# Performance work log

Hardware: AMD Instinct MI355X
Metric: run time of the kernel (lower is better)

## Reference

```python
import jax, jax.numpy as jnp
import numpy as np

N_SRC = 50000
N_DST = 50000
N_EDGES = 500000
HIDDEN = 128
HEADS = 8
HEAD_DIM = HIDDEN // HEADS
SCALE = HEAD_DIM ** -0.5


def setup_inputs() -> dict:
    key = jax.random.key(0)
    ks = jax.random.split(key, 12)
    lim = 1.0 / np.sqrt(HIDDEN)
    def lin(k):
        kw, kb = jax.random.split(k)
        W = jax.random.uniform(kw, (HIDDEN, HIDDEN), jnp.float32, -lim, lim)
        b = jax.random.uniform(kb, (HIDDEN,), jnp.float32, -lim, lim)
        return W, b
    Wq, bq = lin(ks[0]); Wk, bk = lin(ks[1]); Wv, bv = lin(ks[2]); Wo, bo = lin(ks[3])
    return {
        "x_src": jax.random.normal(ks[4], (N_SRC, HIDDEN), jnp.float32),
        "x_dst": jax.random.normal(ks[5], (N_DST, HIDDEN), jnp.float32),
        "edge_index": jax.random.randint(ks[6], (2, N_EDGES), 0, N_SRC, jnp.int64),
        "Wq": Wq, "bq": bq, "Wk": Wk, "bk": bk, "Wv": Wv, "bv": bv,
        "Wo": Wo, "bo": bo,
        "edge_bias": jax.random.normal(ks[7], (HEADS,), jnp.float32) * 0.02,
    }


def reference(x_src, x_dst, edge_index, Wq, bq, Wk, bk, Wv, bv, Wo, bo, edge_bias):
    num_dst = x_dst.shape[0]
    # projections (torch Linear: y = x W^T + b), reshape to (N, H, D)
    q = (x_dst @ Wq.T + bq).reshape(num_dst, HEADS, HEAD_DIM)
    k = (x_src @ Wk.T + bk).reshape(-1, HEADS, HEAD_DIM)
    v = (x_src @ Wv.T + bv).reshape(-1, HEADS, HEAD_DIM)
    src_idx, dst_idx = edge_index[0], edge_index[1]
    # per-edge dot-product scores: (E, H)
    scores = (q[dst_idx] * k[src_idx]).sum(-1) * SCALE + edge_bias
    # sparse softmax over edges grouped by destination
    m = jax.ops.segment_max(scores, dst_idx, num_segments=num_dst)  # (N_dst, H)
    e = jnp.exp(scores - m[dst_idx])
    s = jax.ops.segment_sum(e, dst_idx, num_segments=num_dst)  # (N_dst, H)
    w = e / (s[dst_idx] + 1e-8)  # (E, H)
    # scatter-add aggregate weighted values
    out = jax.ops.segment_sum(w[:, :, None] * v[src_idx], dst_idx, num_segments=num_dst)
    out = out.reshape(num_dst, HIDDEN)
    return out @ Wo.T + bo
```

## Files before the change

### kernel.cpp

```cpp
#include <hip/hip_runtime.h>
#include <math.h>

#define HIDDEN 128
#define SCALE 0.25f
#define NB_G 391

typedef __attribute__((ext_vector_type(8))) short short8v;
typedef __attribute__((ext_vector_type(4))) float f32x4;

__device__ __forceinline__ unsigned short f2bf(float f) {
  const unsigned u = __float_as_uint(f);
  const unsigned r = u + 0x7fffu + ((u >> 16) & 1u);
  return (unsigned short)(r >> 16);
}
__device__ __forceinline__ unsigned pack_bf2(float a, float b) {
  unsigned r;
  asm("v_cvt_pk_bf16_f32 %0, %1, %2" : "=v"(r) : "v"(a), "v"(b));
  return r;
}
__device__ __forceinline__ float bflo(unsigned u) { return __uint_as_float(u << 16); }
__device__ __forceinline__ float bfhi(unsigned u) { return __uint_as_float(u & 0xffff0000u); }

__device__ __forceinline__ void gload_lds16(const void* g, void* l) {
  __builtin_amdgcn_global_load_lds(
      (const __attribute__((address_space(1))) unsigned*)g,
      (__attribute__((address_space(3))) unsigned*)l, 16, 0, 0);
}

__global__ __launch_bounds__(256) void init_kernel(
    const float* __restrict__ W0, const float* __restrict__ W1,
    const float* __restrict__ W2, const float* __restrict__ W3,
    unsigned short* __restrict__ Wfrag, int* __restrict__ zero_base, int nzero4)
{
  if (blockIdx.x < 32) {
    const int chunk = blockIdx.x * 256 + threadIdx.x;
    const int m = chunk >> 11;
    const int rem = chunk & 2047;
    const int l = rem & 63;
    const int nkk = rem >> 6;
    const int n = nkk >> 2, kk = nkk & 3;
    const float* W = (m == 0) ? W0 : (m == 1) ? W1 : (m == 2) ? W2 : W3;
    const int row = n * 16 + (l & 15);
    const int k0 = kk * 32 + (l >> 4) * 8;
    const float4 v0 = *(const float4*)&W[row * 128 + k0];
    const float4 v1 = *(const float4*)&W[row * 128 + k0 + 4];
    uint4 o;
    o.x = (unsigned)f2bf(v0.x) | ((unsigned)f2bf(v0.y) << 16);
    o.y = (unsigned)f2bf(v0.z) | ((unsigned)f2bf(v0.w) << 16);
    o.z = (unsigned)f2bf(v1.x) | ((unsigned)f2bf(v1.y) << 16);
    o.w = (unsigned)f2bf(v1.z) | ((unsigned)f2bf(v1.w) << 16);
    *(uint4*)&Wfrag[(size_t)chunk * 8] = o;
  } else {
    const int idx4 = (blockIdx.x - 32) * 256 + threadIdx.x;
    if (idx4 < nzero4)
      *(int4*)&zero_base[idx4 * 4] = make_int4(0, 0, 0, 0);
  }
}

__global__ __launch_bounds__(256) void count_kernel(
    const int* __restrict__ ei, int E, int* __restrict__ counts)
{
  const int e = (blockIdx.x * 256 + threadIdx.x) * 4;
  if (e + 4 <= E) {
    const int4 d = *(const int4*)&ei[E + e];
    atomicAdd(&counts[d.x], 1);
    atomicAdd(&counts[d.y], 1);
    atomicAdd(&counts[d.z], 1);
    atomicAdd(&counts[d.w], 1);
  } else {
    for (int k = e; k < E; ++k) atomicAdd(&counts[ei[E + k]], 1);
  }
}

__global__ __launch_bounds__(256, 4) void qkv_gemm_kernel(
    const float* __restrict__ x_src, const float* __restrict__ x_dst,
    const unsigned short* __restrict__ Wfrag,
    const float* __restrict__ bq, const float* __restrict__ bk,
    const float* __restrict__ bv,
    unsigned short* __restrict__ qb, unsigned short* __restrict__ kvb,
    int Nsrc, int Ndst)
{
  __shared__ __align__(16) char Xs[2][16384];
  const int t = threadIdx.x;
  const int l = t & 63, w = t >> 6;
  const int r16 = l & 15, g16 = l >> 4;

  int bid = blockIdx.x;
  const float* X; const float* bias; const unsigned short* wbase;
  unsigned short* out; int ostride, ooff, N;
  if (bid < NB_G)        { X = x_src; bias = bk; wbase = Wfrag + 16384; out = kvb; ostride = 256; ooff = 0;   N = Nsrc; }
  else if (bid < 2*NB_G) { bid -= NB_G;   X = x_src; bias = bv; wbase = Wfrag + 32768; out = kvb; ostride = 256; ooff = 128; N = Nsrc; }
  else                   { bid -= 2*NB_G; X = x_dst; bias = bq; wbase = Wfrag;         out = qb;  ostride = 128; ooff = 0;   N = Ndst; }
  const int ntiles = (N + 63) >> 6;

  short8v wfr[2][4];
  #pragma unroll
  for (int cb = 0; cb < 2; ++cb)
    #pragma unroll
    for (int kk = 0; kk < 4; ++kk)
      wfr[cb][kk] = ((const short8v*)wbase)[((w * 2 + cb) * 4 + kk) * 64 + l];
  float4 bb[2];
  #pragma unroll
  for (int cb = 0; cb < 2; ++cb) bb[cb] = *(const float4*)&bias[w * 32 + cb * 16 + g16 * 4];

  float4 xv[8];
  int tile = bid;
  {
    #pragma unroll
    for (int it = 0; it < 8; ++it) {
      const int c = it * 256 + t;
      const int row = c >> 5, fc = (c & 31) << 2;
      const int g = tile * 64 + row;
      xv[it] = make_float4(0.f, 0.f, 0.f, 0.f);
      if (g < N) xv[it] = *(const float4*)&X[(size_t)g * 128 + fc];
    }
    #pragma unroll
    for (int it = 0; it < 8; ++it) {
      const int c = it * 256 + t;
      const int row = c >> 5, b8 = (c & 31) << 3;
      uint2 p;
      p.x = pack_bf2(xv[it].x, xv[it].y);
      p.y = pack_bf2(xv[it].z, xv[it].w);
      *(uint2*)&Xs[0][row * 256 + (b8 ^ ((row & 7) << 4))] = p;
    }
    __syncthreads();
  }

  int cur = 0;
  for (; tile < ntiles; tile += NB_G) {
    const int nt = tile + NB_G;
    if (nt < ntiles) {
      #pragma unroll
      for (int it = 0; it < 8; ++it) {
        const int c = it * 256 + t;
        const int row = c >> 5, fc = (c & 31) << 2;
        const int g = nt * 64 + row;
        xv[it] = make_float4(0.f, 0.f, 0.f, 0.f);
        if (g < N) xv[it] = *(const float4*)&X[(size_t)g * 128 + fc];
      }
    }
    f32x4 acc[4][2];
    #pragma unroll
    for (int rb = 0; rb < 4; ++rb)
      #pragma unroll
      for (int cb = 0; cb < 2; ++cb)
        acc[rb][cb] = (f32x4){bb[cb].x, bb[cb].y, bb[cb].z, bb[cb].w};
    #pragma unroll
    for (int rb = 0; rb < 4; ++rb) {
      const char* ax = &Xs[cur][(rb * 16 + r16) * 256];
      #pragma unroll
      for (int kk = 0; kk < 4; ++kk) {
        const short8v b = *(const short8v*)(ax + (((kk * 32 + g16 * 8) * 2) ^ ((r16 & 7) << 4)));
        acc[rb][0] = __builtin_amdgcn_mfma_f32_16x16x32_bf16(wfr[0][kk], b, acc[rb][0], 0, 0, 0);
        acc[rb][1] = __builtin_amdgcn_mfma_f32_16x16x32_bf16(wfr[1][kk], b, acc[rb][1], 0, 0, 0);
      }
    }
    #pragma unroll
    for (int rb = 0; rb < 4; ++rb) {
      const int g = tile * 64 + rb * 16 + r16;
      if (g < N) {
        unsigned short* orow = out + (size_t)g * ostride + ooff + w * 32;
        #pragma unroll
        for (int cb = 0; cb < 2; ++cb) {
          uint2 o;
          o.x = pack_bf2(acc[rb][cb][0], acc[rb][cb][1]);
          o.y = pack_bf2(acc[rb][cb][2], acc[rb][cb][3]);
          *(uint2*)&orow[cb * 16 + g16 * 4] = o;
        }
      }
    }
    if (nt < ntiles) {
      #pragma unroll
      for (int it = 0; it < 8; ++it) {
        const int c = it * 256 + t;
        const int row = c >> 5, b8 = (c & 31) << 3;
        uint2 p;
        p.x = pack_bf2(xv[it].x, xv[it].y);
        p.y = pack_bf2(xv[it].z, xv[it].w);
        *(uint2*)&Xs[cur ^ 1][row * 256 + (b8 ^ ((row & 7) << 4))] = p;
      }
    }
    __syncthreads();
    cur ^= 1;
  }
}

__global__ __launch_bounds__(256, 4) void out_gemm_kernel(
    const unsigned short* __restrict__ agg, const unsigned short* __restrict__ Wfrag_o,
    const float* __restrict__ bo, float* __restrict__ Y, int N)
{
  __shared__ __align__(16) char Xs[2][16384];
  const int t = threadIdx.x;
  const int l = t & 63, w = t >> 6;
  const int r16 = l & 15, g16 = l >> 4;
  const int ntiles = (N + 63) >> 6;

  short8v wfr[2][4];
  #pragma unroll
  for (int cb = 0; cb < 2; ++cb)
    #pragma unroll
    for (int kk = 0; kk < 4; ++kk)
      wfr[cb][kk] = ((const short8v*)Wfrag_o)[((w * 2 + cb) * 4 + kk) * 64 + l];
  float4 bb[2];
  #pragma unroll
  for (int cb = 0; cb < 2; ++cb) bb[cb] = *(const float4*)&bo[w * 32 + cb * 16 + g16 * 4];

  int tile = blockIdx.x;
  #pragma unroll
  for (int it = 0; it < 4; ++it) {
    const int c = it * 256 + t;
    const int row = c >> 4, c16 = c & 15;
    gload_lds16((const char*)agg + (size_t)(tile * 64 + row) * 256 + ((c16 * 16) ^ ((row & 7) << 4)),
                &Xs[0][c * 16]);
  }
  int cur = 0;
  for (; tile < ntiles; tile += NB_G) {
    const int nt = tile + NB_G;
    asm volatile("s_waitcnt vmcnt(0)" ::: "memory");
    __builtin_amdgcn_sched_barrier(0);
    __syncthreads();
    if (nt < ntiles) {
      #pragma unroll
      for (int it = 0; it < 4; ++it) {
        const int c = it * 256 + t;
        const int row = c >> 4, c16 = c & 15;
        gload_lds16((const char*)agg + (size_t)(nt * 64 + row) * 256 + ((c16 * 16) ^ ((row & 7) << 4)),
                    &Xs[cur ^ 1][c * 16]);
      }
    }
    f32x4 acc[4][2];
    #pragma unroll
    for (int rb = 0; rb < 4; ++rb)
      #pragma unroll
      for (int cb = 0; cb < 2; ++cb)
        acc[rb][cb] = (f32x4){bb[cb].x, bb[cb].y, bb[cb].z, bb[cb].w};
    #pragma unroll
    for (int rb = 0; rb < 4; ++rb) {
      const char* ax = &Xs[cur][(rb * 16 + r16) * 256];
      #pragma unroll
      for (int kk = 0; kk < 4; ++kk) {
        const short8v b = *(const short8v*)(ax + (((kk * 32 + g16 * 8) * 2) ^ ((r16 & 7) << 4)));
        acc[rb][0] = __builtin_amdgcn_mfma_f32_16x16x32_bf16(wfr[0][kk], b, acc[rb][0], 0, 0, 0);
        acc[rb][1] = __builtin_amdgcn_mfma_f32_16x16x32_bf16(wfr[1][kk], b, acc[rb][1], 0, 0, 0);
      }
    }
    #pragma unroll
    for (int rb = 0; rb < 4; ++rb) {
      const int g = tile * 64 + rb * 16 + r16;
      if (g < N) {
        float* yrow = Y + (size_t)g * 128 + w * 32;
        #pragma unroll
        for (int cb = 0; cb < 2; ++cb)
          *(float4*)&yrow[cb * 16 + g16 * 4] =
              make_float4(acc[rb][cb][0], acc[rb][cb][1], acc[rb][cb][2], acc[rb][cb][3]);
      }
    }
    cur ^= 1;
  }
}

__global__ __launch_bounds__(256) void scan_fused_kernel(
    const int* __restrict__ counts, int n, int* __restrict__ bsums,
    int* __restrict__ done, int* __restrict__ offsets)
{
  const int b = blockIdx.x, t = threadIdx.x;
  const int lane = t & 63, wid = t >> 6;
  const int idx = b * 256 + t;
  const int x = (idx < n) ? counts[idx] : 0;
  int v = x;
  #pragma unroll
  for (int off = 1; off < 64; off <<= 1) {
    const int tmp = __shfl_up(v, off);
    if (lane >= off) v += tmp;
  }
  __shared__ int wsum[4];
  __shared__ int base_s;
  if (lane == 63) wsum[wid] = v;
  __syncthreads();
  if (t == 0) {
    bsums[b] = wsum[0] + wsum[1] + wsum[2] + wsum[3];
    __threadfence();
    atomicAdd(done, 1);
    while (atomicAdd(done, 0) < (int)gridDim.x) {}
  }
  __syncthreads();
  __threadfence();
  int pre = (t < b) ? bsums[t] : 0;
  #pragma unroll
  for (int off = 1; off < 64; off <<= 1) pre += __shfl_xor(pre, off);
  __shared__ int pres[4];
  if (lane == 0) pres[wid] = pre;
  __syncthreads();
  if (t == 0) base_s = pres[0] + pres[1] + pres[2] + pres[3];
  __syncthreads();
  int wbase = 0;
  for (int p = 0; p < wid; ++p) wbase += wsum[p];
  if (idx < n) offsets[idx] = base_s + wbase + v - x;
}

__global__ __launch_bounds__(256) void scatter_kernel(
    const int* __restrict__ ei, int E, int* __restrict__ offsets,
    int* __restrict__ csr_src)
{
  const int e = (blockIdx.x * 256 + threadIdx.x) * 4;
  if (e + 4 <= E) {
    const int4 s = *(const int4*)&ei[e];
    const int4 d = *(const int4*)&ei[E + e];
    int p;
    p = atomicAdd(&offsets[d.x], 1); csr_src[p] = s.x;
    p = atomicAdd(&offsets[d.y], 1); csr_src[p] = s.y;
    p = atomicAdd(&offsets[d.z], 1); csr_src[p] = s.z;
    p = atomicAdd(&offsets[d.w], 1); csr_src[p] = s.w;
  } else {
    for (int k = e; k < E; ++k) {
      const int d = ei[E + k];
      const int p = atomicAdd(&offsets[d], 1);
      csr_src[p] = ei[k];
    }
  }
}

__global__ __launch_bounds__(256) void edge_attn_kernel(
    const unsigned short* __restrict__ qb, const unsigned short* __restrict__ kvb,
    const float* __restrict__ eb, const int* __restrict__ offsets,
    const int* __restrict__ counts, const int* __restrict__ csr_src,
    unsigned short* __restrict__ agg, int Ndst)
{
  const int wave = blockIdx.x * 4 + (threadIdx.x >> 6);
  if (wave >= Ndst) return;
  const int lane = threadIdx.x & 63;
  const int eg = lane >> 3, h = lane & 7;

  const uint4 q0 = *(const uint4*)&qb[(size_t)wave * 128 + h * 16];
  const uint4 q1 = *(const uint4*)&qb[(size_t)wave * 128 + h * 16 + 8];
  const float bias = eb[h];
  const int ro = (wave == 0) ? 0 : offsets[wave - 1];
  const int cnt = counts[wave];

  float acc[16];
  #pragma unroll
  for (int j = 0; j < 16; ++j) acc[j] = 0.f;
  float s = 0.f;

  int e = eg;
  bool act = e < cnt;
  int src = act ? csr_src[ro + e] : 0;
  const int iters = (cnt + 7) >> 3;
  for (int it = 0; it < iters; ++it) {
    const size_t base = (size_t)src * 256 + h * 16;
    const uint4 k0 = *(const uint4*)&kvb[base];
    const uint4 k1 = *(const uint4*)&kvb[base + 8];
    const uint4 v0 = *(const uint4*)&kvb[base + 128];
    const uint4 v1 = *(const uint4*)&kvb[base + 136];
    const int e2 = e + 8;
    const bool act2 = e2 < cnt;
    const int src2 = act2 ? csr_src[ro + e2] : 0;

    float p = 0.f;
    p = fmaf(bflo(q0.x), bflo(k0.x), p); p = fmaf(bfhi(q0.x), bfhi(k0.x), p);
    p = fmaf(bflo(q0.y), bflo(k0.y), p); p = fmaf(bfhi(q0.y), bfhi(k0.y), p);
    p = fmaf(bflo(q0.z), bflo(k0.z), p); p = fmaf(bfhi(q0.z), bfhi(k0.z), p);
    p = fmaf(bflo(q0.w), bflo(k0.w), p); p = fmaf(bfhi(q0.w), bfhi(k0.w), p);
    p = fmaf(bflo(q1.x), bflo(k1.x), p); p = fmaf(bfhi(q1.x), bfhi(k1.x), p);
    p = fmaf(bflo(q1.y), bflo(k1.y), p); p = fmaf(bfhi(q1.y), bfhi(k1.y), p);
    p = fmaf(bflo(q1.z), bflo(k1.z), p); p = fmaf(bfhi(q1.z), bfhi(k1.z), p);
    p = fmaf(bflo(q1.w), bflo(k1.w), p); p = fmaf(bfhi(q1.w), bfhi(k1.w), p);

    const float wgt = act ? __expf(fmaf(p, SCALE, bias)) : 0.f;
    s += wgt;
    acc[0]  = fmaf(wgt, bflo(v0.x), acc[0]);  acc[1]  = fmaf(wgt, bfhi(v0.x), acc[1]);
    acc[2]  = fmaf(wgt, bflo(v0.y), acc[2]);  acc[3]  = fmaf(wgt, bfhi(v0.y), acc[3]);
    acc[4]  = fmaf(wgt, bflo(v0.z), acc[4]);  acc[5]  = fmaf(wgt, bfhi(v0.z), acc[5]);
    acc[6]  = fmaf(wgt, bflo(v0.w), acc[6]);  acc[7]  = fmaf(wgt, bfhi(v0.w), acc[7]);
    acc[8]  = fmaf(wgt, bflo(v1.x), acc[8]);  acc[9]  = fmaf(wgt, bfhi(v1.x), acc[9]);
    acc[10] = fmaf(wgt, bflo(v1.y), acc[10]); acc[11] = fmaf(wgt, bfhi(v1.y), acc[11]);
    acc[12] = fmaf(wgt, bflo(v1.z), acc[12]); acc[13] = fmaf(wgt, bfhi(v1.z), acc[13]);
    acc[14] = fmaf(wgt, bflo(v1.w), acc[14]); acc[15] = fmaf(wgt, bfhi(v1.w), acc[15]);
    e = e2; act = act2; src = src2;
  }

  const bool b0 = eg & 1, b1 = (eg >> 1) & 1, b2 = (eg >> 2) & 1;
  float r8[8];
  #pragma unroll
  for (int j = 0; j < 8; ++j) {
    const float keep = b0 ? acc[j + 8] : acc[j];
    const float send = b0 ? acc[j] : acc[j + 8];
    r8[j] = keep + __shfl_xor(send, 8);
  }
  float r4[4];
  #pragma unroll
  for (int j = 0; j < 4; ++j) {
    const float keep = b1 ? r8[j + 2] : r8[j];
    const float send = b1 ? r8[j] : r8[j + 2];
    r4[j] = keep + __shfl_xor(send, 16);
  }
  float r4b[4];
  #pragma unroll
  for (int j = 0; j < 4; ++j) {
    const float keep = b1 ? r8[j + 4] : r8[j];
    const float send = b1 ? r8[j] : r8[j + 4];
    r4b[j] = keep + __shfl_xor(send, 16);
  }
  float r2[2];
  #pragma unroll
  for (int j = 0; j < 2; ++j) {
    const float keep = b2 ? r4b[j + 2] : r4b[j];
    const float send = b2 ? r4b[j] : r4b[j + 2];
    r2[j] = keep + __shfl_xor(send, 32);
  }
  s += __shfl_xor(s, 8); s += __shfl_xor(s, 16); s += __shfl_xor(s, 32);
  const float rs = 1.0f / (s + 1e-8f);
  const int col = h * 16 + (b0 ? 8 : 0) + (b1 ? 4 : 0) + (b2 ? 2 : 0);
  *(unsigned*)&agg[(size_t)wave * 128 + col] = pack_bf2(r2[0] * rs, r2[1] * rs);
}

extern "C" void kernel_launch(void* const* d_in, const int* in_sizes, int n_in,
                              void* d_out, int out_size, void* d_ws, size_t ws_size,
                              hipStream_t stream) {
  const float* x_src = (const float*)d_in[0];
  const float* x_dst = (const float*)d_in[1];
  const int*   ei    = (const int*)d_in[2];
  const float* Wq = (const float*)d_in[3];
  const float* bq = (const float*)d_in[4];
  const float* Wk = (const float*)d_in[5];
  const float* bk = (const float*)d_in[6];
  const float* Wv = (const float*)d_in[7];
  const float* bv = (const float*)d_in[8];
  const float* Wo = (const float*)d_in[9];
  const float* bo = (const float*)d_in[10];
  const float* eb = (const float*)d_in[11];

  const int Nsrc = in_sizes[0] / HIDDEN;
  const int Ndst = in_sizes[1] / HIDDEN;
  const int E    = in_sizes[2] / 2;

  char* w = (char*)d_ws;
  unsigned short* qb   = (unsigned short*)w; w += (size_t)Ndst * 128 * 2;
  unsigned short* kvb  = (unsigned short*)w; w += (size_t)Nsrc * 256 * 2;
  unsigned short* aggb = (unsigned short*)w; w += (size_t)Ndst * 128 * 2;
  unsigned short* Wb   = (unsigned short*)w; w += (size_t)4 * 16384 * 2;
  int* counts  = (int*)w; w += (size_t)Ndst * sizeof(int);
  int* done    = (int*)w; w += 64 * sizeof(int);
  int* offsets = (int*)w; w += (size_t)Ndst * sizeof(int);
  int* bsums   = (int*)w; w += 256 * sizeof(int);
  int* csr_src = (int*)w; w += (size_t)E * sizeof(int);

  dim3 blk256(256);
  const int nzero4 = (Ndst + 64 + 3) / 4;
  const int zblocks = (nzero4 + 255) / 256;
  init_kernel<<<32 + zblocks, blk256, 0, stream>>>(Wq, Wk, Wv, Wo, Wb, counts, nzero4);

  const int e4blocks = (E / 4 + 255) / 256;
  count_kernel<<<e4blocks, blk256, 0, stream>>>(ei, E, counts);

  qkv_gemm_kernel<<<3 * NB_G, blk256, 0, stream>>>(
      x_src, x_dst, Wb, bq, bk, bv, qb, kvb, Nsrc, Ndst);

  const int nb = (Ndst + 255) / 256;
  scan_fused_kernel<<<nb, blk256, 0, stream>>>(counts, Ndst, bsums, done, offsets);

  scatter_kernel<<<e4blocks, blk256, 0, stream>>>(ei, E, offsets, csr_src);

  const int ablocks = (Ndst + 3) / 4;
  edge_attn_kernel<<<ablocks, blk256, 0, stream>>>(qb, kvb, eb, offsets, counts,
                                                   csr_src, aggb, Ndst);

  out_gemm_kernel<<<NB_G, blk256, 0, stream>>>(aggb, Wb + 49152, bo, (float*)d_out, Ndst);
}
```

Measured before the change: 157.5 us.

## Restructure projection GEMMs per-wave with LDS weights and fold count into QKV launch

The QKV and output GEMMs now stage the full bf16 weight matrix in LDS once per block. Each wave owns a 16-row tile, loads its X rows straight into registers as MFMA operands and computes all 128 output columns. This removes the per-tile LDS staging of X and the block-wide barriers of the old double-buffered scheme. The degree-count atomics move into extra blocks of the QKV launch, saving one kernel launch. An unused shuffle-reduction branch in the attention kernel is also dropped. The cost is more LDS reads of weight fragments per MFMA, and a lower block count that may reduce latency hiding.

```diff
diff --git a/kernel.cpp b/kernel.cpp
--- a/kernel.cpp
+++ b/kernel.cpp
@@ -3,7 +3,7 @@
 
 #define HIDDEN 128
 #define SCALE 0.25f
-#define NB_G 391
+#define NB_F 256
 
 typedef __attribute__((ext_vector_type(8))) short short8v;
 typedef __attribute__((ext_vector_type(4))) float f32x4;
@@ -57,131 +57,113 @@
   }
 }
 
-__global__ __launch_bounds__(256) void count_kernel(
-    const int* __restrict__ ei, int E, int* __restrict__ counts)
-{
-  const int e = (blockIdx.x * 256 + threadIdx.x) * 4;
-  if (e + 4 <= E) {
-    const int4 d = *(const int4*)&ei[E + e];
-    atomicAdd(&counts[d.x], 1);
-    atomicAdd(&counts[d.y], 1);
-    atomicAdd(&counts[d.z], 1);
-    atomicAdd(&counts[d.w], 1);
-  } else {
-    for (int k = e; k < E; ++k) atomicAdd(&counts[ei[E + k]], 1);
-  }
-}
-
-__global__ __launch_bounds__(256, 4) void qkv_gemm_kernel(
+__global__ __launch_bounds__(256, 4) void qkv_count_kernel(
     const float* __restrict__ x_src, const float* __restrict__ x_dst,
     const unsigned short* __restrict__ Wfrag,
     const float* __restrict__ bq, const float* __restrict__ bk,
     const float* __restrict__ bv,
     unsigned short* __restrict__ qb, unsigned short* __restrict__ kvb,
-    int Nsrc, int Ndst)
-{
-  __shared__ __align__(16) char Xs[2][16384];
+    int Nsrc, int Ndst,
+    const int* __restrict__ ei, int E, int* __restrict__ counts)
+{
+  __shared__ __align__(16) char WsB[32768];
+  __shared__ float bias_s[128];
   const int t = threadIdx.x;
+  const int bid = blockIdx.x;
+
+  if (bid >= 3 * NB_F) {
+    const int e = ((bid - 3 * NB_F) * 256 + t) * 4;
+    if (e + 4 <= E) {
+      const int4 d = *(const int4*)&ei[E + e];
+      atomicAdd(&counts[d.x], 1);
+      atomicAdd(&counts[d.y], 1);
+      atomicAdd(&counts[d.z], 1);
+      atomicAdd(&counts[d.w], 1);
+    } else {
+      for (int k = e; k < E; ++k) atomicAdd(&counts[ei[E + k]], 1);
+    }
+    return;
+  }
+
+  const int flavor = bid / NB_F, sub = bid % NB_F;
+  const float* X; const float* bias; const unsigned short* wbase;
+  unsigned short* out; int ostride, ooff, N;
+  if (flavor == 0)      { X = x_src; bias = bk; wbase = Wfrag + 16384; out = kvb; ostride = 256; ooff = 0;   N = Nsrc; }
+  else if (flavor == 1) { X = x_src; bias = bv; wbase = Wfrag + 32768; out = kvb; ostride = 256; ooff = 128; N = Nsrc; }
+  else                  { X = x_dst; bias = bq; wbase = Wfrag;         out = qb;  ostride = 128; ooff = 0;   N = Ndst; }
+
+  #pragma unroll
+  for (int it = 0; it < 8; ++it) {
+    const int off = (it * 256 + t) * 16;
+    gload_lds16((const char*)wbase + off, WsB + off);
+  }
+  if (t < 128) bias_s[t] = bias[t];
+  asm volatile("s_waitcnt vmcnt(0)" ::: "memory");
+  __syncthreads();
+
   const int l = t & 63, w = t >> 6;
   const int r16 = l & 15, g16 = l >> 4;
-
-  int bid = blockIdx.x;
-  const float* X; const float* bias; const unsigned short* wbase;
-  unsigned short* out; int ostride, ooff, N;
-  if (bid < NB_G)        { X = x_src; bias = bk; wbase = Wfrag + 16384; out = kvb; ostride = 256; ooff = 0;   N = Nsrc; }
-  else if (bid < 2*NB_G) { bid -= NB_G;   X = x_src; bias = bv; wbase = Wfrag + 32768; out = kvb; ostride = 256; ooff = 128; N = Nsrc; }
-  else                   { bid -= 2*NB_G; X = x_dst; bias = bq; wbase = Wfrag;         out = qb;  ostride = 128; ooff = 0;   N = Ndst; }
-  const int ntiles = (N + 63) >> 6;
-
-  short8v wfr[2][4];
-  #pragma unroll
-  for (int cb = 0; cb < 2; ++cb)
-    #pragma unroll
-    for (int kk = 0; kk < 4; ++kk)
-      wfr[cb][kk] = ((const short8v*)wbase)[((w * 2 + cb) * 4 + kk) * 64 + l];
-  float4 bb[2];
-  #pragma unroll
-  for (int cb = 0; cb < 2; ++cb) bb[cb] = *(const float4*)&bias[w * 32 + cb * 16 + g16 * 4];
+  const int ntiles = (N + 15) >> 4;
+  const int stride = NB_F * 4;
+  int tile = sub * 4 + w;
+  if (tile >= ntiles) return;
 
   float4 xv[8];
-  int tile = bid;
   {
-    #pragma unroll
-    for (int it = 0; it < 8; ++it) {
-      const int c = it * 256 + t;
-      const int row = c >> 5, fc = (c & 31) << 2;
-      const int g = tile * 64 + row;
-      xv[it] = make_float4(0.f, 0.f, 0.f, 0.f);
-      if (g < N) xv[it] = *(const float4*)&X[(size_t)g * 128 + fc];
-    }
-    #pragma unroll
-    for (int it = 0; it < 8; ++it) {
-      const int c = it * 256 + t;
-      const int row = c >> 5, b8 = (c & 31) << 3;
-      uint2 p;
-      p.x = pack_bf2(xv[it].x, xv[it].y);
-      p.y = pack_bf2(xv[it].z, xv[it].w);
-      *(uint2*)&Xs[0][row * 256 + (b8 ^ ((row & 7) << 4))] = p;
-    }
-    __syncthreads();
-  }
-
-  int cur = 0;
-  for (; tile < ntiles; tile += NB_G) {
-    const int nt = tile + NB_G;
+    const int row = tile * 16 + r16;
+    const bool valid = row < N;
+    const float* xp = X + (size_t)row * 128 + g16 * 8;
+    #pragma unroll
+    for (int kk = 0; kk < 4; ++kk) {
+      xv[2 * kk]     = valid ? *(const float4*)(xp + kk * 32)     : make_float4(0.f, 0.f, 0.f, 0.f);
+      xv[2 * kk + 1] = valid ? *(const float4*)(xp + kk * 32 + 4) : make_float4(0.f, 0.f, 0.f, 0.f);
+    }
+  }
+  for (; tile < ntiles; tile += stride) {
+    const int nt = tile + stride;
+    short8v a[4];
+    #pragma unroll
+    for (int kk = 0; kk < 4; ++kk) {
+      uint4 u;
+      u.x = pack_bf2(xv[2 * kk].x,     xv[2 * kk].y);
+      u.y = pack_bf2(xv[2 * kk].z,     xv[2 * kk].w);
+      u.z = pack_bf2(xv[2 * kk + 1].x, xv[2 * kk + 1].y);
+      u.w = pack_bf2(xv[2 * kk + 1].z, xv[2 * kk + 1].w);
+      a[kk] = *(short8v*)&u;
+    }
     if (nt < ntiles) {
-      #pragma unroll
-      for (int it = 0; it < 8; ++it) {
-        const int c = it * 256 + t;
-        const int row = c >> 5, fc = (c & 31) << 2;
-        const int g = nt * 64 + row;
-        xv[it] = make_float4(0.f, 0.f, 0.f, 0.f);
-        if (g < N) xv[it] = *(const float4*)&X[(size_t)g * 128 + fc];
+      const int row = nt * 16 + r16;
+      const bool valid = row < N;
+      const float* xp = X + (size_t)row * 128 + g16 * 8;
+      #pragma unroll
+      for (int kk = 0; kk < 4; ++kk) {
+        xv[2 * kk]     = valid ? *(const float4*)(xp + kk * 32)     : make_float4(0.f, 0.f, 0.f, 0.f);
+        xv[2 * kk + 1] = valid ? *(const float4*)(xp + kk * 32 + 4) : make_float4(0.f, 0.f, 0.f, 0.f);
       }
     }
-    f32x4 acc[4][2];
-    #pragma unroll
-    for (int rb = 0; rb < 4; ++rb)
-      #pragma unroll
-      for (int cb = 0; cb < 2; ++cb)
-        acc[rb][cb] = (f32x4){bb[cb].x, bb[cb].y, bb[cb].z, bb[cb].w};
-    #pragma unroll
-    for (int rb = 0; rb < 4; ++rb) {
-      const char* ax = &Xs[cur][(rb * 16 + r16) * 256];
-      #pragma unroll
-      for (int kk = 0; kk < 4; ++kk) {
-        const short8v b = *(const short8v*)(ax + (((kk * 32 + g16 * 8) * 2) ^ ((r16 & 7) << 4)));
-        acc[rb][0] = __builtin_amdgcn_mfma_f32_16x16x32_bf16(wfr[0][kk], b, acc[rb][0], 0, 0, 0);
-        acc[rb][1] = __builtin_amdgcn_mfma_f32_16x16x32_bf16(wfr[1][kk], b, acc[rb][1], 0, 0, 0);
+    f32x4 acc[8];
+    #pragma unroll
+    for (int n = 0; n < 8; ++n) acc[n] = (f32x4){0.f, 0.f, 0.f, 0.f};
+    #pragma unroll
+    for (int kk = 0; kk < 4; ++kk) {
+      #pragma unroll
+      for (int n = 0; n < 8; ++n) {
+        const short8v wf = *(const short8v*)&WsB[((n * 4 + kk) * 64 + l) * 16];
+        acc[n] = __builtin_amdgcn_mfma_f32_16x16x32_bf16(wf, a[kk], acc[n], 0, 0, 0);
       }
     }
-    #pragma unroll
-    for (int rb = 0; rb < 4; ++rb) {
-      const int g = tile * 64 + rb * 16 + r16;
-      if (g < N) {
-        unsigned short* orow = out + (size_t)g * ostride + ooff + w * 32;
-        #pragma unroll
-        for (int cb = 0; cb < 2; ++cb) {
-          uint2 o;
-          o.x = pack_bf2(acc[rb][cb][0], acc[rb][cb][1]);
-          o.y = pack_bf2(acc[rb][cb][2], acc[rb][cb][3]);
-          *(uint2*)&orow[cb * 16 + g16 * 4] = o;
-        }
+    const int row = tile * 16 + r16;
+    if (row < N) {
+      unsigned short* orow = out + (size_t)row * ostride + ooff;
+      #pragma unroll
+      for (int n = 0; n < 8; ++n) {
+        const float4 bb = *(const float4*)&bias_s[n * 16 + g16 * 4];
+        uint2 o;
+        o.x = pack_bf2(acc[n][0] + bb.x, acc[n][1] + bb.y);
+        o.y = pack_bf2(acc[n][2] + bb.z, acc[n][3] + bb.w);
+        *(uint2*)&orow[n * 16 + g16 * 4] = o;
       }
     }
-    if (nt < ntiles) {
-      #pragma unroll
-      for (int it = 0; it < 8; ++it) {
-        const int c = it * 256 + t;
-        const int row = c >> 5, b8 = (c & 31) << 3;
-        uint2 p;
-        p.x = pack_bf2(xv[it].x, xv[it].y);
-        p.y = pack_bf2(xv[it].z, xv[it].w);
-        *(uint2*)&Xs[cur ^ 1][row * 256 + (b8 ^ ((row & 7) << 4))] = p;
-      }
-    }
-    __syncthreads();
-    cur ^= 1;
   }
 }
 
@@ -189,73 +171,68 @@
     const unsigned short* __restrict__ agg, const unsigned short* __restrict__ Wfrag_o,
     const float* __restrict__ bo, float* __restrict__ Y, int N)
 {
-  __shared__ __align__(16) char Xs[2][16384];
+  __shared__ __align__(16) char WsB[32768];
+  __shared__ float bias_s[128];
   const int t = threadIdx.x;
+  #pragma unroll
+  for (int it = 0; it < 8; ++it) {
+    const int off = (it * 256 + t) * 16;
+    gload_lds16((const char*)Wfrag_o + off, WsB + off);
+  }
+  if (t < 128) bias_s[t] = bo[t];
+  asm volatile("s_waitcnt vmcnt(0)" ::: "memory");
+  __syncthreads();
+
   const int l = t & 63, w = t >> 6;
   const int r16 = l & 15, g16 = l >> 4;
-  const int ntiles = (N + 63) >> 6;
-
-  short8v wfr[2][4];
-  #pragma unroll
-  for (int cb = 0; cb < 2; ++cb)
+  const int ntiles = (N + 15) >> 4;
+  const int stride = NB_F * 4;
+  int tile = blockIdx.x * 4 + w;
+  if (tile >= ntiles) return;
+
+  uint4 av[4];
+  {
+    const int row = tile * 16 + r16;
+    const bool valid = row < N;
+    const unsigned short* ap = agg + (size_t)row * 128 + g16 * 8;
     #pragma unroll
     for (int kk = 0; kk < 4; ++kk)
-      wfr[cb][kk] = ((const short8v*)Wfrag_o)[((w * 2 + cb) * 4 + kk) * 64 + l];
-  float4 bb[2];
-  #pragma unroll
-  for (int cb = 0; cb < 2; ++cb) bb[cb] = *(const float4*)&bo[w * 32 + cb * 16 + g16 * 4];
-
-  int tile = blockIdx.x;
-  #pragma unroll
-  for (int it = 0; it < 4; ++it) {
-    const int c = it * 256 + t;
-    const int row = c >> 4, c16 = c & 15;
-    gload_lds16((const char*)agg + (size_t)(tile * 64 + row) * 256 + ((c16 * 16) ^ ((row & 7) << 4)),
-                &Xs[0][c * 16]);
-  }
-  int cur = 0;
-  for (; tile < ntiles; tile += NB_G) {
-    const int nt = tile + NB_G;
-    asm volatile("s_waitcnt vmcnt(0)" ::: "memory");
-    __builtin_amdgcn_sched_barrier(0);
-    __syncthreads();
+      av[kk] = valid ? *(const uint4*)(ap + kk * 32) : make_uint4(0, 0, 0, 0);
+  }
+  for (; tile < ntiles; tile += stride) {
+    const int nt = tile + stride;
+    short8v a[4];
+    #pragma unroll
+    for (int kk = 0; kk < 4; ++kk) a[kk] = *(short8v*)&av[kk];
     if (nt < ntiles) {
-      #pragma unroll
-      for (int it = 0; it < 4; ++it) {
-        const int c = it * 256 + t;
-        const int row = c >> 4, c16 = c & 15;
-        gload_lds16((const char*)agg + (size_t)(nt * 64 + row) * 256 + ((c16 * 16) ^ ((row & 7) << 4)),
-                    &Xs[cur ^ 1][c * 16]);
+      const int row = nt * 16 + r16;
+      const bool valid = row < N;
+      const unsigned short* ap = agg + (size_t)row * 128 + g16 * 8;
+      #pragma unroll
+      for (int kk = 0; kk < 4; ++kk)
+        av[kk] = valid ? *(const uint4*)(ap + kk * 32) : make_uint4(0, 0, 0, 0);
+    }
+    f32x4 acc[8];
+    #pragma unroll
+    for (int n = 0; n < 8; ++n) acc[n] = (f32x4){0.f, 0.f, 0.f, 0.f};
+    #pragma unroll
+    for (int kk = 0; kk < 4; ++kk) {
+      #pragma unroll
+      for (int n = 0; n < 8; ++n) {
+        const short8v wf = *(const short8v*)&WsB[((n * 4 + kk) * 64 + l) * 16];
+        acc[n] = __builtin_amdgcn_mfma_f32_16x16x32_bf16(wf, a[kk], acc[n], 0, 0, 0);
       }
     }
-    f32x4 acc[4][2];
-    #pragma unroll
-    for (int rb = 0; rb < 4; ++rb)
-      #pragma unroll
-      for (int cb = 0; cb < 2; ++cb)
-        acc[rb][cb] = (f32x4){bb[cb].x, bb[cb].y, bb[cb].z, bb[cb].w};
-    #pragma unroll
-    for (int rb = 0; rb < 4; ++rb) {
-      const char* ax = &Xs[cur][(rb * 16 + r16) * 256];
-      #pragma unroll
-      for (int kk = 0; kk < 4; ++kk) {
-        const short8v b = *(const short8v*)(ax + (((kk * 32 + g16 * 8) * 2) ^ ((r16 & 7) << 4)));
-        acc[rb][0] = __builtin_amdgcn_mfma_f32_16x16x32_bf16(wfr[0][kk], b, acc[rb][0], 0, 0, 0);
-        acc[rb][1] = __builtin_amdgcn_mfma_f32_16x16x32_bf16(wfr[1][kk], b, acc[rb][1], 0, 0, 0);
+    const int row = tile * 16 + r16;
+    if (row < N) {
+      float* yrow = Y + (size_t)row * 128;
+      #pragma unroll
+      for (int n = 0; n < 8; ++n) {
+        const float4 bb = *(const float4*)&bias_s[n * 16 + g16 * 4];
+        *(float4*)&yrow[n * 16 + g16 * 4] =
+            make_float4(acc[n][0] + bb.x, acc[n][1] + bb.y, acc[n][2] + bb.z, acc[n][3] + bb.w);
       }
     }
-    #pragma unroll
-    for (int rb = 0; rb < 4; ++rb) {
-      const int g = tile * 64 + rb * 16 + r16;
-      if (g < N) {
-        float* yrow = Y + (size_t)g * 128 + w * 32;
-        #pragma unroll
-        for (int cb = 0; cb < 2; ++cb)
-          *(float4*)&yrow[cb * 16 + g16 * 4] =
-              make_float4(acc[rb][cb][0], acc[rb][cb][1], acc[rb][cb][2], acc[rb][cb][3]);
-      }
-    }
-    cur ^= 1;
   }
 }
 
@@ -390,22 +367,15 @@
   float r4[4];
   #pragma unroll
   for (int j = 0; j < 4; ++j) {
-    const float keep = b1 ? r8[j + 2] : r8[j];
-    const float send = b1 ? r8[j] : r8[j + 2];
-    r4[j] = keep + __shfl_xor(send, 16);
-  }
-  float r4b[4];
-  #pragma unroll
-  for (int j = 0; j < 4; ++j) {
     const float keep = b1 ? r8[j + 4] : r8[j];
     const float send = b1 ? r8[j] : r8[j + 4];
-    r4b[j] = keep + __shfl_xor(send, 16);
+    r4[j] = keep + __shfl_xor(send, 16);
   }
   float r2[2];
   #pragma unroll
   for (int j = 0; j < 2; ++j) {
-    const float keep = b2 ? r4b[j + 2] : r4b[j];
-    const float send = b2 ? r4b[j] : r4b[j + 2];
+    const float keep = b2 ? r4[j + 2] : r4[j];
+    const float send = b2 ? r4[j] : r4[j + 2];
     r2[j] = keep + __shfl_xor(send, 32);
   }
   s += __shfl_xor(s, 8); s += __shfl_xor(s, 16); s += __shfl_xor(s, 32);
@@ -451,10 +421,8 @@
   init_kernel<<<32 + zblocks, blk256, 0, stream>>>(Wq, Wk, Wv, Wo, Wb, counts, nzero4);
 
   const int e4blocks = (E / 4 + 255) / 256;
-  count_kernel<<<e4blocks, blk256, 0, stream>>>(ei, E, counts);
-
-  qkv_gemm_kernel<<<3 * NB_G, blk256, 0, stream>>>(
-      x_src, x_dst, Wb, bq, bk, bv, qb, kvb, Nsrc, Ndst);
+  qkv_count_kernel<<<3 * NB_F + e4blocks, blk256, 0, stream>>>(
+      x_src, x_dst, Wb, bq, bk, bv, qb, kvb, Nsrc, Ndst, ei, E, counts);
 
   const int nb = (Ndst + 255) / 256;
   scan_fused_kernel<<<nb, blk256, 0, stream>>>(counts, Ndst, bsums, done, offsets);
@@ -465,5 +433,5 @@
   edge_attn_kernel<<<ablocks, blk256, 0, stream>>>(qb, kvb, eb, offsets, counts,
                                                    csr_src, aggb, Ndst);
 
-  out_gemm_kernel<<<NB_G, blk256, 0, stream>>>(aggb, Wb + 49152, bo, (float*)d_out, Ndst);
-}
+  out_gemm_kernel<<<NB_F, blk256, 0, stream>>>(aggb, Wb + 49152, bo, (float*)d_out, Ndst);
+}
```

Result: faster. 153.9 us (-2.3%).
